# Optimization experiments

Measured on AMD Instinct MI355X. Metric: run time of the kernel, lower is better.

## Reference

```python
import jax, jax.numpy as jnp
import numpy as np

T = 2048          # tokens (single-sequence prefill)
HID = 4096        # hidden_size
NH = 32           # num attention heads
NKV = 8           # num kv heads (GQA)
HD = 128          # head_dim
QKV_OUT = (NH + 2 * NKV) * HD  # 6144
THETA = 10000.0
SCALING = HD ** -0.5


def setup_inputs() -> dict:
    key = jax.random.key(0)
    ks = jax.random.split(key, 8)
    positions = jnp.arange(T, dtype=jnp.int32)
    # per-token int8 quantized hidden states (symmetric, [-127,127])
    q_act = jax.random.randint(ks[0], (T, HID), -127, 128, dtype=jnp.int32)
    # per-token dynamic activation scale
    act_scale = jax.random.uniform(ks[1], (T,), jnp.float32) * 0.01 + 0.001
    # int4 weights stored unsigned [0,15] with per-output-channel scale & zero point
    w_qkv_q = jax.random.randint(ks[2], (QKV_OUT, HID), 0, 16, dtype=jnp.int32)
    w_qkv_scale = jax.random.uniform(ks[3], (QKV_OUT,), jnp.float32) * 0.01 + 0.001
    w_qkv_zero = jax.random.uniform(ks[4], (QKV_OUT,), jnp.float32) * 2.0 + 7.0
    w_o_q = jax.random.randint(ks[5], (HID, HID), 0, 16, dtype=jnp.int32)
    w_o_scale = jax.random.uniform(ks[6], (HID,), jnp.float32) * 0.01 + 0.001
    w_o_zero = jax.random.uniform(ks[7], (HID,), jnp.float32) * 2.0 + 7.0
    return dict(positions=positions, q_act=q_act, act_scale=act_scale,
                w_qkv_q=w_qkv_q, w_qkv_scale=w_qkv_scale, w_qkv_zero=w_qkv_zero,
                w_o_q=w_o_q, w_o_scale=w_o_scale, w_o_zero=w_o_zero)


def w4a8_linear(qa_f, s_a, a_sum, qw, s_w, z_w):
    # y[t,o] = s_a[t]*s_w[o] * ( (qa @ qw^T)[t,o] - z_w[o]*sum_j qa[t,j] )
    acc = jnp.matmul(qa_f, qw.astype(jnp.float32).T)  # [T, O]
    return (s_a[:, None] * s_w[None, :]) * (acc - z_w[None, :] * a_sum[:, None])


def apply_rope(x, positions):
    # neox-style RoPE over full head_dim
    half = HD // 2
    inv_freq = THETA ** (-jnp.arange(0, half, dtype=jnp.float32) / half * 1.0)
    inv_freq = 1.0 / (THETA ** (jnp.arange(0, HD, 2, dtype=jnp.float32) / HD))
    freqs = positions.astype(jnp.float32)[:, None] * inv_freq[None, :]  # [T, HD/2]
    cos = jnp.cos(freqs)[:, None, :]
    sin = jnp.sin(freqs)[:, None, :]
    x1, x2 = x[..., :half], x[..., half:]
    return jnp.concatenate([x1 * cos - x2 * sin, x2 * cos + x1 * sin], axis=-1)


def dynamic_quant_with_sum(x):
    # per-token symmetric int8 dynamic quantization + fused sum
    s = jnp.maximum(jnp.max(jnp.abs(x), axis=-1), 1e-8) / 127.0  # [T]
    q = jnp.clip(jnp.round(x / s[:, None]), -127, 127)
    return q, s, jnp.sum(q, axis=-1)


def reference(positions, q_act, act_scale, w_qkv_q, w_qkv_scale, w_qkv_zero,
              w_o_q, w_o_scale, w_o_zero):
    qa_f = q_act.astype(jnp.float32)
    a_sum = jnp.sum(qa_f, axis=-1)  # fused activation sum
    qkv = w4a8_linear(qa_f, act_scale, a_sum, w_qkv_q, w_qkv_scale, w_qkv_zero)
    q, k, v = jnp.split(qkv, [NH * HD, NH * HD + NKV * HD], axis=-1)
    q = q.reshape(T, NH, HD)
    k = k.reshape(T, NKV, HD)
    v = v.reshape(T, NKV, HD)
    q = apply_rope(q, positions)
    k = apply_rope(k, positions)
    # GQA: repeat kv heads
    rep = NH // NKV
    k = jnp.repeat(k, rep, axis=1)  # [T, NH, HD]
    v = jnp.repeat(v, rep, axis=1)
    scores = jnp.einsum('qhd,khd->hqk', q, k) * SCALING  # [NH, T, T]
    causal = jnp.tril(jnp.ones((T, T), dtype=bool))
    scores = jnp.where(causal[None], scores, -jnp.inf)
    probs = jax.nn.softmax(scores, axis=-1)
    attn = jnp.einsum('hqk,khd->qhd', probs, v).reshape(T, NH * HD)
    # invoke_quant_fuse_sum: dynamic per-token quantization of attn output
    q2, s2, sum2 = dynamic_quant_with_sum(attn)
    out = w4a8_linear(q2, s2, sum2, w_o_q, w_o_scale, w_o_zero)
    return out
```

## Files before the change

kernel.cpp:

```cpp
#include <hip/hip_runtime.h>

#define T 2048
#define HID 4096
#define NH 32
#define NKV 8
#define HD 128
#define QKV_OUT ((NH + 2*NKV) * HD)
#define SCALING 0.08838834764831843f
#define ROPE_C 0.20762050593046014f

typedef __attribute__((ext_vector_type(8))) short bfrag;
typedef __attribute__((ext_vector_type(4))) float ffrag;
typedef __attribute__((ext_vector_type(4))) int  ifrag;
typedef __attribute__((ext_vector_type(16))) char c16;

__device__ __forceinline__ short f2bf(float f) {
  unsigned u = __builtin_bit_cast(unsigned, f);
  u += 0x7fffu + ((u >> 16) & 1u);
  return (short)(u >> 16);
}

__device__ __forceinline__ void split2(float x, short& hi, short& lo) {
  unsigned u = __builtin_bit_cast(unsigned, x);
  unsigned uh = u + (0x7fffu + ((u >> 16) & 1u));
  hi = (short)(uh >> 16);
  float fh = __builtin_bit_cast(float, uh & 0xffff0000u);
  float r = x - fh;
  unsigned ur = __builtin_bit_cast(unsigned, r);
  ur += 0x7fffu + ((ur >> 16) & 1u);
  lo = (short)(ur >> 16);
}

__device__ __forceinline__ void gload_lds16(const void* g, void* l) {
  __builtin_amdgcn_global_load_lds(
      (const __attribute__((address_space(1))) unsigned int*)g,
      (__attribute__((address_space(3))) unsigned int*)l, 16, 0, 0);
}

__global__ __launch_bounds__(256)
void asum_conv(const int* __restrict__ qact, float* __restrict__ a_sum,
               char* __restrict__ a_i8) {
  __shared__ int red[256];
  const int t = blockIdx.x, tid = threadIdx.x;
  const int* row = qact + (size_t)t * HID + tid * 16;
  int s = 0;
  c16 o;
#pragma unroll
  for (int i = 0; i < 4; i++) {
    int4 v = *(const int4*)(row + i * 4);
    s += v.x + v.y + v.z + v.w;
    o[i*4+0] = (char)v.x; o[i*4+1] = (char)v.y;
    o[i*4+2] = (char)v.z; o[i*4+3] = (char)v.w;
  }
  *(c16*)(a_i8 + (size_t)t * HID + tid * 16) = o;
  red[tid] = s; __syncthreads();
  for (int off = 128; off > 0; off >>= 1) {
    if (tid < off) red[tid] += red[tid + off];
    __syncthreads();
  }
  if (tid == 0) a_sum[t] = (float)red[0];
}

__global__ __launch_bounds__(256)
void conv_i2c(const int* __restrict__ src, char* __restrict__ dst, int n16) {
  int idx = blockIdx.x * 256 + threadIdx.x;
  if (idx >= n16) return;
  const int4* s4 = (const int4*)src + (size_t)idx * 4;
  c16 o;
#pragma unroll
  for (int j = 0; j < 4; j++) {
    int4 v = s4[j];
    o[j*4+0] = (char)v.x; o[j*4+1] = (char)v.y;
    o[j*4+2] = (char)v.z; o[j*4+3] = (char)v.w;
  }
  *(c16*)(dst + (size_t)idx * 16) = o;
}

__global__ __launch_bounds__(256)
void gemm_i8(const char* __restrict__ A, const char* __restrict__ W,
             const float* __restrict__ s_a, const float* __restrict__ asum,
             const float* __restrict__ s_w, const float* __restrict__ z_w,
             float* __restrict__ C, int M, int N, int K) {
  __shared__ __align__(16) char As[128 * 64];
  __shared__ __align__(16) char Bs[128 * 64];
  const int tid = threadIdx.x;
  const int lane = tid & 63;
  const int quad = lane >> 4, l15 = lane & 15;
  const int wave = tid >> 6;
  const int wm = (wave >> 1) * 64, wn = (wave & 1) * 64;
  const int bm = blockIdx.y * 128, bn = blockIdx.x * 128;
  const int sr = tid >> 2, sc = (tid & 3) * 16;

  ifrag acc[4][4];
#pragma unroll
  for (int mi = 0; mi < 4; mi++)
#pragma unroll
    for (int ni = 0; ni < 4; ni++)
      acc[mi][ni] = (ifrag){0, 0, 0, 0};

  for (int k0 = 0; k0 < K; k0 += 64) {
#pragma unroll
    for (int it = 0; it < 2; it++) {
      gload_lds16(A + (size_t)(bm + it * 64 + sr) * K + k0 + sc,
                  &As[it * 4096 + wave * 1024]);
      gload_lds16(W + (size_t)(bn + it * 64 + sr) * K + k0 + sc,
                  &Bs[it * 4096 + wave * 1024]);
    }
    __syncthreads();

    ifrag af[4], bfv[4];
#pragma unroll
    for (int mi = 0; mi < 4; mi++)
      af[mi] = *(const ifrag*)&As[(wm + mi * 16 + l15) * 64 + quad * 16];
#pragma unroll
    for (int ni = 0; ni < 4; ni++)
      bfv[ni] = *(const ifrag*)&Bs[(wn + ni * 16 + l15) * 64 + quad * 16];
#pragma unroll
    for (int mi = 0; mi < 4; mi++)
#pragma unroll
      for (int ni = 0; ni < 4; ni++)
        acc[mi][ni] = __builtin_amdgcn_mfma_i32_16x16x64_i8(
            af[mi], bfv[ni], acc[mi][ni], 0, 0, 0);
    __syncthreads();
  }

#pragma unroll
  for (int mi = 0; mi < 4; mi++) {
    int row0 = bm + wm + mi * 16 + quad * 4;
#pragma unroll
    for (int r = 0; r < 4; r++) {
      int row = row0 + r;
      float sa = s_a[row], av = asum[row];
#pragma unroll
      for (int ni = 0; ni < 4; ni++) {
        int col = bn + wn + ni * 16 + l15;
        C[(size_t)row * N + col] = (sa * s_w[col]) * ((float)acc[mi][ni][r] - z_w[col] * av);
      }
    }
  }
}

__global__ __launch_bounds__(256)
void split_kv(float* __restrict__ qkv, const int* __restrict__ positions,
              short* __restrict__ Kh, short* __restrict__ Kl,
              short* __restrict__ Vth) {
  __shared__ __align__(16) short Vh_lds[128 * 72];
  const int y = blockIdx.y;
  const int t0 = blockIdx.x * 64;
  const int tid = threadIdx.x;

  if (y >= NKV) {
    const int h = y - NKV;
#pragma unroll
    for (int it = 0; it < 4; it++) {
      int c = tid + 256 * it;
      int key = c >> 4, dc = c & 15;
      float* qr = qkv + (size_t)(t0 + key) * QKV_OUT + (size_t)h * HD;
      float4 a = *(const float4*)(qr + dc * 4);
      float4 b = *(const float4*)(qr + dc * 4 + 64);
      float av[4] = {a.x, a.y, a.z, a.w};
      float bv[4] = {b.x, b.y, b.z, b.w};
      float pos = (float)positions[t0 + key];
#pragma unroll
      for (int jj = 0; jj < 4; jj++) {
        float fr = pos * exp2f(-ROPE_C * (float)(dc * 4 + jj));
        float sn, cs; sincosf(fr, &sn, &cs);
        float x1 = av[jj], x2 = bv[jj];
        av[jj] = x1 * cs - x2 * sn;
        bv[jj] = x2 * cs + x1 * sn;
      }
      *(float4*)(qr + dc * 4)      = make_float4(av[0], av[1], av[2], av[3]);
      *(float4*)(qr + dc * 4 + 64) = make_float4(bv[0], bv[1], bv[2], bv[3]);
    }
    return;
  }

  const int kvh = y;
#pragma unroll
  for (int it = 0; it < 4; it++) {
    int c = tid + 256 * it;
    int key = c >> 4, dc = c & 15;
    const float* kr = qkv + (size_t)(t0 + key) * QKV_OUT
                      + (size_t)NH * HD + (size_t)kvh * HD;
    float4 a = *(const float4*)(kr + dc * 4);
    float4 b = *(const float4*)(kr + dc * 4 + 64);
    float av[4] = {a.x, a.y, a.z, a.w};
    float bv[4] = {b.x, b.y, b.z, b.w};
    float pos = (float)positions[t0 + key];
    short4 ha, la, hb, lb;
    short hh, ll;
#pragma unroll
    for (int jj = 0; jj < 4; jj++) {
      float fr = pos * exp2f(-ROPE_C * (float)(dc * 4 + jj));
      float sn, cs; sincosf(fr, &sn, &cs);
      float x1 = av[jj], x2 = bv[jj];
      float r1 = x1 * cs - x2 * sn;
      float r2 = x2 * cs + x1 * sn;
      split2(r1, hh, ll); ((short*)&ha)[jj] = hh; ((short*)&la)[jj] = ll;
      split2(r2, hh, ll); ((short*)&hb)[jj] = hh; ((short*)&lb)[jj] = ll;
    }
    size_t o1 = (size_t)kvh * T * HD + (size_t)(t0 + key) * HD + dc * 4;
    *(short4*)(Kh + o1) = ha;      *(short4*)(Kl + o1) = la;
    *(short4*)(Kh + o1 + 64) = hb; *(short4*)(Kl + o1 + 64) = lb;
  }
#pragma unroll
  for (int i = 0; i < 8; i++) {
    int c = tid + 256 * i;
    int key = c >> 5, dc = c & 31;
    float4 f = *(const float4*)(qkv + (size_t)(t0 + key) * QKV_OUT
                                + (size_t)(NH + NKV) * HD + (size_t)kvh * HD + dc * 4);
    Vh_lds[(dc*4+0)*72 + key] = f2bf(f.x);
    Vh_lds[(dc*4+1)*72 + key] = f2bf(f.y);
    Vh_lds[(dc*4+2)*72 + key] = f2bf(f.z);
    Vh_lds[(dc*4+3)*72 + key] = f2bf(f.w);
  }
  __syncthreads();
#pragma unroll
  for (int i = 0; i < 2; i++) {
    int c = tid + 256 * i;
    int row = c >> 2, cc = c & 3;
    size_t o = (size_t)kvh * HD * T + (size_t)row * T + t0 + cc * 8;
    *(bfrag*)(Vth + o) = *(const bfrag*)&Vh_lds[row * 72 + cc * 8];
  }
#pragma unroll
  for (int i = 0; i < 2; i++) {
    int c = tid + 256 * i;
    int row = c >> 2, cc = c & 3;
    size_t o = (size_t)kvh * HD * T + (size_t)row * T + t0 + 32 + cc * 8;
    *(bfrag*)(Vth + o) = *(const bfrag*)&Vh_lds[row * 72 + 32 + cc * 8];
  }
}

__global__ __launch_bounds__(256)
void attn_kernel(const float* __restrict__ qkv,
                 const short* __restrict__ Kh, const short* __restrict__ Kl,
                 const short* __restrict__ Vth,
                 float* __restrict__ Opart, float* __restrict__ Mp,
                 float* __restrict__ Lp, float* __restrict__ attn) {
  __shared__ __align__(16) short Ksh[32 * 136];
  __shared__ __align__(16) short Ksl[32 * 136];
  __shared__ __align__(16) short Vsh[128 * 40];
  __shared__ __align__(16) short Psh[4 * 16 * 40];

  const int kvh = blockIdx.y;
  const int pair = blockIdx.x >> 1;
  const int half = blockIdx.x & 1;
  const int tid = threadIdx.x;
  const int lane = tid & 63;
  const int wv = tid >> 6;
  const int l15 = lane & 15, quad = lane >> 4;
  const int h = kvh * 4 + wv;
  short* Pw = Psh + wv * 16 * 40;

  const short* KhB = Kh + (size_t)kvh * T * HD;
  const short* KlB = Kl + (size_t)kvh * T * HD;
  const short* VhB = Vth + (size_t)kvh * HD * T;

  const int kr = tid >> 4, kc8 = (tid & 15) * 8;
  const int vd = tid >> 2, vc8 = (tid & 3) * 8;

  bfrag rkh0, rkh1, rkl0, rkl1, rv0, rv1;
  auto preload = [&](int k0) {
    rkh0 = *(const bfrag*)(KhB + (size_t)(k0 + kr) * HD + kc8);
    rkh1 = *(const bfrag*)(KhB + (size_t)(k0 + kr + 16) * HD + kc8);
    rkl0 = *(const bfrag*)(KlB + (size_t)(k0 + kr) * HD + kc8);
    rkl1 = *(const bfrag*)(KlB + (size_t)(k0 + kr + 16) * HD + kc8);
    rv0  = *(const bfrag*)(VhB + (size_t)vd * T + k0 + vc8);
    rv1  = *(const bfrag*)(VhB + (size_t)(vd + 64) * T + k0 + vc8);
  };
  preload(half * 32);

  bfrag ones;
#pragma unroll
  for (int j = 0; j < 8; j++) ones[j] = (short)0x3f80;

  for (int pass = 0; pass < 2; pass++) {
    const int qt = pass ? pair : 127 - pair;
    const int q0 = qt * 16;
    const int nk = (q0 >> 5) + 1;

    bfrag qh[4], ql[4];
    const float* qrow = qkv + (size_t)(q0 + l15) * QKV_OUT + (size_t)h * HD;
#pragma unroll
    for (int kc = 0; kc < 4; kc++) {
      float4 f0 = *(const float4*)(qrow + kc * 32 + quad * 8);
      float4 f1 = *(const float4*)(qrow + kc * 32 + quad * 8 + 4);
      float fv[8] = {f0.x, f0.y, f0.z, f0.w, f1.x, f1.y, f1.z, f1.w};
#pragma unroll
      for (int j = 0; j < 8; j++) {
        short hi, lo; split2(fv[j], hi, lo);
        qh[kc][j] = hi; ql[kc][j] = lo;
      }
    }

    ffrag o[8], ol;
    ol = (ffrag){0.f, 0.f, 0.f, 0.f};
#pragma unroll
    for (int n = 0; n < 8; n++) o[n] = (ffrag){0.f, 0.f, 0.f, 0.f};
    float m_i[4] = {-1e30f, -1e30f, -1e30f, -1e30f};

    for (int kt = half; kt < nk; kt += 2) {
      const int k0 = kt << 5;
      __syncthreads();
      *(bfrag*)&Ksh[kr * 136 + kc8] = rkh0;
      *(bfrag*)&Ksh[(kr + 16) * 136 + kc8] = rkh1;
      *(bfrag*)&Ksl[kr * 136 + kc8] = rkl0;
      *(bfrag*)&Ksl[(kr + 16) * 136 + kc8] = rkl1;
      *(bfrag*)&Vsh[vd * 40 + vc8] = rv0;
      *(bfrag*)&Vsh[(vd + 64) * 40 + vc8] = rv1;
      if (kt + 2 < nk) preload(k0 + 64);
      else if (pass == 0) preload(half * 32);
      __syncthreads();

      ffrag s[2];
      s[0] = (ffrag){0.f,0.f,0.f,0.f}; s[1] = (ffrag){0.f,0.f,0.f,0.f};
#pragma unroll
      for (int n = 0; n < 2; n++) {
#pragma unroll
        for (int kc = 0; kc < 4; kc++) {
          bfrag bh = *(const bfrag*)&Ksh[(n*16 + l15) * 136 + kc*32 + quad*8];
          bfrag bl = *(const bfrag*)&Ksl[(n*16 + l15) * 136 + kc*32 + quad*8];
          s[n] = __builtin_amdgcn_mfma_f32_16x16x32_bf16(qh[kc], bh, s[n], 0,0,0);
          s[n] = __builtin_amdgcn_mfma_f32_16x16x32_bf16(qh[kc], bl, s[n], 0,0,0);
          s[n] = __builtin_amdgcn_mfma_f32_16x16x32_bf16(ql[kc], bh, s[n], 0,0,0);
        }
      }
      const bool last = (kt == nk - 1);
      float sv[2][4];
#pragma unroll
      for (int n = 0; n < 2; n++)
#pragma unroll
        for (int r = 0; r < 4; r++) {
          float v = s[n][r] * SCALING;
          if (last) {
            int key = k0 + n * 16 + l15;
            int row = q0 + quad * 4 + r;
            if (key > row) v = -1e30f;
          }
          sv[n][r] = v;
        }
      float alpha[4];
      bool anyup = false;
#pragma unroll
      for (int r = 0; r < 4; r++) {
        float mt = fmaxf(sv[0][r], sv[1][r]);
        mt = fmaxf(mt, __shfl_xor(mt, 1));
        mt = fmaxf(mt, __shfl_xor(mt, 2));
        mt = fmaxf(mt, __shfl_xor(mt, 4));
        mt = fmaxf(mt, __shfl_xor(mt, 8));
        float m_new = fmaxf(m_i[r], mt);
        alpha[r] = __expf(m_i[r] - m_new);
        if (m_new > m_i[r]) anyup = true;
        m_i[r] = m_new;
      }
#pragma unroll
      for (int n = 0; n < 2; n++)
#pragma unroll
        for (int r = 0; r < 4; r++) {
          float p = __expf(sv[n][r] - m_i[r]);
          Pw[(quad*4 + r) * 40 + n*16 + l15] = f2bf(p);
        }
      if (__any(anyup)) {
#pragma unroll
        for (int r = 0; r < 4; r++) ol[r] *= alpha[r];
#pragma unroll
        for (int n = 0; n < 8; n++)
#pragma unroll
          for (int r = 0; r < 4; r++) o[n][r] *= alpha[r];
      }
      bfrag ph = *(const bfrag*)&Pw[l15 * 40 + quad * 8];
      ol = __builtin_amdgcn_mfma_f32_16x16x32_bf16(ph, ones, ol, 0,0,0);
#pragma unroll
      for (int n = 0; n < 8; n++) {
        bfrag vh = *(const bfrag*)&Vsh[(n*16 + l15) * 40 + quad * 8];
        o[n] = __builtin_amdgcn_mfma_f32_16x16x32_bf16(ph, vh, o[n], 0,0,0);
      }
    }

    float* dst = half ? attn : Opart;
#pragma unroll
    for (int n = 0; n < 8; n++)
#pragma unroll
      for (int r = 0; r < 4; r++) {
        int row = q0 + quad * 4 + r;
        dst[(size_t)row * HID + (size_t)h * HD + n * 16 + l15] = o[n][r];
      }
    if (l15 == 0) {
#pragma unroll
      for (int r = 0; r < 4; r++) {
        int row = q0 + quad * 4 + r;
        size_t ix = (size_t)half * NH * T + (size_t)h * T + row;
        Mp[ix] = m_i[r];
        Lp[ix] = ol[r];
      }
    }
  }
}

__global__ __launch_bounds__(256)
void attn_combine(const float* __restrict__ Opart, const float* __restrict__ Mp,
                  const float* __restrict__ Lp, float* attn) {
  const int row = blockIdx.x, tid = threadIdx.x;
  const int h = tid >> 3;
  const float m0 = Mp[(size_t)h * T + row];
  const float m1 = Mp[(size_t)NH * T + (size_t)h * T + row];
  const float l0 = Lp[(size_t)h * T + row];
  const float l1 = Lp[(size_t)NH * T + (size_t)h * T + row];
  const float m = fmaxf(m0, m1);
  float s0 = __expf(m0 - m), s1 = __expf(m1 - m);
  const float inv = 1.f / (l0 * s0 + l1 * s1);
  s0 *= inv; s1 *= inv;
  const size_t base = (size_t)row * HID + (size_t)tid * 16;
  float4* dst = (float4*)(attn + base);
  const float4* p0 = (const float4*)(Opart + base);
#pragma unroll
  for (int i = 0; i < 4; i++) {
    float4 a = p0[i];
    float4 b = dst[i];
    dst[i] = make_float4(a.x * s0 + b.x * s1, a.y * s0 + b.y * s1,
                         a.z * s0 + b.z * s1, a.w * s0 + b.w * s1);
  }
}

__global__ __launch_bounds__(256)
void quant_kernel(const float* __restrict__ x, char* __restrict__ q2,
                  float* __restrict__ s2, float* __restrict__ sum2) {
  __shared__ float red[256];
  const int t = blockIdx.x, tid = threadIdx.x;
  const float* row = x + (size_t)t * HID;
  float4 v[4];
  float m = 0.f;
#pragma unroll
  for (int i = 0; i < 4; i++) {
    v[i] = *(const float4*)(row + tid * 16 + i * 4);
    m = fmaxf(m, fmaxf(fmaxf(fabsf(v[i].x), fabsf(v[i].y)),
                       fmaxf(fabsf(v[i].z), fabsf(v[i].w))));
  }
  red[tid] = m; __syncthreads();
  for (int off = 128; off > 0; off >>= 1) {
    if (tid < off) red[tid] = fmaxf(red[tid], red[tid + off]);
    __syncthreads();
  }
  float s = fmaxf(red[0], 1e-8f) / 127.f;
  __syncthreads();
  float ssum = 0.f;
  c16 o;
#pragma unroll
  for (int i = 0; i < 4; i++) {
    float q;
    q = fminf(127.f, fmaxf(-127.f, rintf(v[i].x / s))); ssum += q; o[i*4+0] = (char)(int)q;
    q = fminf(127.f, fmaxf(-127.f, rintf(v[i].y / s))); ssum += q; o[i*4+1] = (char)(int)q;
    q = fminf(127.f, fmaxf(-127.f, rintf(v[i].z / s))); ssum += q; o[i*4+2] = (char)(int)q;
    q = fminf(127.f, fmaxf(-127.f, rintf(v[i].w / s))); ssum += q; o[i*4+3] = (char)(int)q;
  }
  *(c16*)(q2 + (size_t)t * HID + tid * 16) = o;
  red[tid] = ssum; __syncthreads();
  for (int off = 128; off > 0; off >>= 1) {
    if (tid < off) red[tid] += red[tid + off];
    __syncthreads();
  }
  if (tid == 0) { s2[t] = s; sum2[t] = red[0]; }
}

extern "C" void kernel_launch(void* const* d_in, const int* in_sizes, int n_in,
                              void* d_out, int out_size, void* d_ws, size_t ws_size,
                              hipStream_t stream) {
  const int*   positions   = (const int*)d_in[0];
  const int*   q_act       = (const int*)d_in[1];
  const float* act_scale   = (const float*)d_in[2];
  const int*   w_qkv_q     = (const int*)d_in[3];
  const float* w_qkv_scale = (const float*)d_in[4];
  const float* w_qkv_zero  = (const float*)d_in[5];
  const int*   w_o_q       = (const int*)d_in[6];
  const float* w_o_scale   = (const float*)d_in[7];
  const float* w_o_zero    = (const float*)d_in[8];
  float* out = (float*)d_out;

  size_t off = 0;
  auto alloc = [&](size_t bytes) -> void* {
    void* p = (char*)d_ws + off;
    off += (bytes + 255) & ~(size_t)255;
    return p;
  };
  float* qkv   = (float*)alloc((size_t)T * QKV_OUT * 4);
  char*  act8  = (char*)alloc((size_t)T * HID);
  char*  w8    = (char*)alloc((size_t)QKV_OUT * HID);
  short* Kh    = (short*)alloc((size_t)NKV * T * HD * 2);
  short* Kl    = (short*)alloc((size_t)NKV * T * HD * 2);
  short* Vth   = (short*)alloc((size_t)NKV * T * HD * 2);
  float* a_sum = (float*)alloc(T * 4);
  float* s2    = (float*)alloc(T * 4);
  float* sum2  = (float*)alloc(T * 4);
  float* Mp    = (float*)alloc((size_t)2 * NH * T * 4);
  float* Lp    = (float*)alloc((size_t)2 * NH * T * 4);
  float* Opart = (float*)act8;
  (void)ws_size;

  asum_conv<<<T, 256, 0, stream>>>(q_act, a_sum, act8);
  conv_i2c<<<(QKV_OUT * HID / 16 + 255) / 256, 256, 0, stream>>>(
      w_qkv_q, w8, QKV_OUT * HID / 16);
  gemm_i8<<<dim3(QKV_OUT / 128, T / 128), 256, 0, stream>>>(
      act8, w8, act_scale, a_sum, w_qkv_scale, w_qkv_zero, qkv, T, QKV_OUT, HID);
  split_kv<<<dim3(T / 64, NKV + NH), 256, 0, stream>>>(qkv, positions, Kh, Kl, Vth);
  attn_kernel<<<dim3(128, NKV), 256, 0, stream>>>(
      qkv, Kh, Kl, Vth, Opart, Mp, Lp, out);
  attn_combine<<<T, 256, 0, stream>>>(Opart, Mp, Lp, out);
  conv_i2c<<<(HID * HID / 16 + 255) / 256, 256, 0, stream>>>(
      w_o_q, w8, HID * HID / 16);
  quant_kernel<<<T, 256, 0, stream>>>(out, act8, s2, sum2);
  gemm_i8<<<dim3(HID / 128, T / 128), 256, 0, stream>>>(
      act8, w8, s2, sum2, w_o_scale, w_o_zero, out, T, HID, HID);
}
```

Before: 562.8 us.

## Split attention grid per q-tile, fold scaling into log2 domain, defer rescaling

Each attention block now handles a single 16-row query tile instead of a paired long/short tile, which doubles the grid to 256x8 blocks for more parallelism at the cost of less even per-block work. Q is prescaled by SCALING*log2(e) so that exp2f replaces __expf and the per-score multiply goes away. The online-softmax rescale of the accumulators now happens only when the tile max exceeds the running max by a threshold, which trades some fp32 overflow headroom for fewer rescales. The Q low-part fragments move to LDS to reduce register pressure.

```diff
diff --git a/kernel.cpp b/kernel.cpp
--- a/kernel.cpp
+++ b/kernel.cpp
@@ -7,6 +7,8 @@
 #define HD 128
 #define QKV_OUT ((NH + 2*NKV) * HD)
 #define SCALING 0.08838834764831843f
+#define QS2 0.12751744954f
+#define DEFER_THR 10.0f
 #define ROPE_C 0.20762050593046014f
 
 typedef __attribute__((ext_vector_type(8))) short bfrag;
@@ -241,9 +243,10 @@
   __shared__ __align__(16) short Ksl[32 * 136];
   __shared__ __align__(16) short Vsh[128 * 40];
   __shared__ __align__(16) short Psh[4 * 16 * 40];
+  __shared__ __align__(16) short Qlo[4 * 4 * 512];
 
   const int kvh = blockIdx.y;
-  const int pair = blockIdx.x >> 1;
+  const int qt  = 127 - (int)(blockIdx.x >> 1);
   const int half = blockIdx.x & 1;
   const int tid = threadIdx.x;
   const int lane = tid & 63;
@@ -274,125 +277,126 @@
 #pragma unroll
   for (int j = 0; j < 8; j++) ones[j] = (short)0x3f80;
 
-  for (int pass = 0; pass < 2; pass++) {
-    const int qt = pass ? pair : 127 - pair;
-    const int q0 = qt * 16;
-    const int nk = (q0 >> 5) + 1;
-
-    bfrag qh[4], ql[4];
-    const float* qrow = qkv + (size_t)(q0 + l15) * QKV_OUT + (size_t)h * HD;
+  const int q0 = qt * 16;
+  const int nk = (q0 >> 5) + 1;
+
+  bfrag qh[4];
+  const float* qrow = qkv + (size_t)(q0 + l15) * QKV_OUT + (size_t)h * HD;
+#pragma unroll
+  for (int kc = 0; kc < 4; kc++) {
+    float4 f0 = *(const float4*)(qrow + kc * 32 + quad * 8);
+    float4 f1 = *(const float4*)(qrow + kc * 32 + quad * 8 + 4);
+    float fv[8] = {f0.x, f0.y, f0.z, f0.w, f1.x, f1.y, f1.z, f1.w};
+    bfrag qhv, qlv;
+#pragma unroll
+    for (int j = 0; j < 8; j++) {
+      short hi, lo; split2(fv[j] * QS2, hi, lo);
+      qhv[j] = hi; qlv[j] = lo;
+    }
+    qh[kc] = qhv;
+    *(bfrag*)&Qlo[(wv * 4 + kc) * 512 + lane * 8] = qlv;
+  }
+
+  ffrag o[8], ol;
+  ol = (ffrag){0.f, 0.f, 0.f, 0.f};
+#pragma unroll
+  for (int n = 0; n < 8; n++) o[n] = (ffrag){0.f, 0.f, 0.f, 0.f};
+  float m_i[4] = {-1e30f, -1e30f, -1e30f, -1e30f};
+
+  for (int kt = half; kt < nk; kt += 2) {
+    const int k0 = kt << 5;
+    __syncthreads();
+    *(bfrag*)&Ksh[kr * 136 + kc8] = rkh0;
+    *(bfrag*)&Ksh[(kr + 16) * 136 + kc8] = rkh1;
+    *(bfrag*)&Ksl[kr * 136 + kc8] = rkl0;
+    *(bfrag*)&Ksl[(kr + 16) * 136 + kc8] = rkl1;
+    *(bfrag*)&Vsh[vd * 40 + vc8] = rv0;
+    *(bfrag*)&Vsh[(vd + 64) * 40 + vc8] = rv1;
+    if (kt + 2 < nk) preload(k0 + 64);
+    __syncthreads();
+
+    ffrag s[2];
+    s[0] = (ffrag){0.f,0.f,0.f,0.f}; s[1] = (ffrag){0.f,0.f,0.f,0.f};
 #pragma unroll
     for (int kc = 0; kc < 4; kc++) {
-      float4 f0 = *(const float4*)(qrow + kc * 32 + quad * 8);
-      float4 f1 = *(const float4*)(qrow + kc * 32 + quad * 8 + 4);
-      float fv[8] = {f0.x, f0.y, f0.z, f0.w, f1.x, f1.y, f1.z, f1.w};
-#pragma unroll
-      for (int j = 0; j < 8; j++) {
-        short hi, lo; split2(fv[j], hi, lo);
-        qh[kc][j] = hi; ql[kc][j] = lo;
+      bfrag qlv = *(const bfrag*)&Qlo[(wv * 4 + kc) * 512 + lane * 8];
+#pragma unroll
+      for (int n = 0; n < 2; n++) {
+        bfrag bh = *(const bfrag*)&Ksh[(n*16 + l15) * 136 + kc*32 + quad*8];
+        bfrag bl = *(const bfrag*)&Ksl[(n*16 + l15) * 136 + kc*32 + quad*8];
+        s[n] = __builtin_amdgcn_mfma_f32_16x16x32_bf16(qh[kc], bh, s[n], 0,0,0);
+        s[n] = __builtin_amdgcn_mfma_f32_16x16x32_bf16(qh[kc], bl, s[n], 0,0,0);
+        s[n] = __builtin_amdgcn_mfma_f32_16x16x32_bf16(qlv,    bh, s[n], 0,0,0);
       }
     }
-
-    ffrag o[8], ol;
-    ol = (ffrag){0.f, 0.f, 0.f, 0.f};
-#pragma unroll
-    for (int n = 0; n < 8; n++) o[n] = (ffrag){0.f, 0.f, 0.f, 0.f};
-    float m_i[4] = {-1e30f, -1e30f, -1e30f, -1e30f};
-
-    for (int kt = half; kt < nk; kt += 2) {
-      const int k0 = kt << 5;
-      __syncthreads();
-      *(bfrag*)&Ksh[kr * 136 + kc8] = rkh0;
-      *(bfrag*)&Ksh[(kr + 16) * 136 + kc8] = rkh1;
-      *(bfrag*)&Ksl[kr * 136 + kc8] = rkl0;
-      *(bfrag*)&Ksl[(kr + 16) * 136 + kc8] = rkl1;
-      *(bfrag*)&Vsh[vd * 40 + vc8] = rv0;
-      *(bfrag*)&Vsh[(vd + 64) * 40 + vc8] = rv1;
-      if (kt + 2 < nk) preload(k0 + 64);
-      else if (pass == 0) preload(half * 32);
-      __syncthreads();
-
-      ffrag s[2];
-      s[0] = (ffrag){0.f,0.f,0.f,0.f}; s[1] = (ffrag){0.f,0.f,0.f,0.f};
-#pragma unroll
-      for (int n = 0; n < 2; n++) {
-#pragma unroll
-        for (int kc = 0; kc < 4; kc++) {
-          bfrag bh = *(const bfrag*)&Ksh[(n*16 + l15) * 136 + kc*32 + quad*8];
-          bfrag bl = *(const bfrag*)&Ksl[(n*16 + l15) * 136 + kc*32 + quad*8];
-          s[n] = __builtin_amdgcn_mfma_f32_16x16x32_bf16(qh[kc], bh, s[n], 0,0,0);
-          s[n] = __builtin_amdgcn_mfma_f32_16x16x32_bf16(qh[kc], bl, s[n], 0,0,0);
-          s[n] = __builtin_amdgcn_mfma_f32_16x16x32_bf16(ql[kc], bh, s[n], 0,0,0);
+    const bool lastkt = (kt == nk - 1);
+    float sv[2][4];
+#pragma unroll
+    for (int n = 0; n < 2; n++)
+#pragma unroll
+      for (int r = 0; r < 4; r++) {
+        float v = s[n][r];
+        if (lastkt) {
+          int key = k0 + n * 16 + l15;
+          int row = q0 + quad * 4 + r;
+          if (key > row) v = -1e30f;
         }
+        sv[n][r] = v;
       }
-      const bool last = (kt == nk - 1);
-      float sv[2][4];
-#pragma unroll
-      for (int n = 0; n < 2; n++)
-#pragma unroll
-        for (int r = 0; r < 4; r++) {
-          float v = s[n][r] * SCALING;
-          if (last) {
-            int key = k0 + n * 16 + l15;
-            int row = q0 + quad * 4 + r;
-            if (key > row) v = -1e30f;
-          }
-          sv[n][r] = v;
-        }
-      float alpha[4];
-      bool anyup = false;
+    float mt[4];
+    bool trig = false;
+#pragma unroll
+    for (int r = 0; r < 4; r++) {
+      float m2 = fmaxf(sv[0][r], sv[1][r]);
+      m2 = fmaxf(m2, __shfl_xor(m2, 1));
+      m2 = fmaxf(m2, __shfl_xor(m2, 2));
+      m2 = fmaxf(m2, __shfl_xor(m2, 4));
+      m2 = fmaxf(m2, __shfl_xor(m2, 8));
+      mt[r] = m2;
+      trig = trig || (m2 > m_i[r] + DEFER_THR);
+    }
+    if (__any(trig)) {
 #pragma unroll
       for (int r = 0; r < 4; r++) {
-        float mt = fmaxf(sv[0][r], sv[1][r]);
-        mt = fmaxf(mt, __shfl_xor(mt, 1));
-        mt = fmaxf(mt, __shfl_xor(mt, 2));
-        mt = fmaxf(mt, __shfl_xor(mt, 4));
-        mt = fmaxf(mt, __shfl_xor(mt, 8));
-        float m_new = fmaxf(m_i[r], mt);
-        alpha[r] = __expf(m_i[r] - m_new);
-        if (m_new > m_i[r]) anyup = true;
-        m_i[r] = m_new;
+        float mn = fmaxf(m_i[r], mt[r]);
+        float a = exp2f(m_i[r] - mn);
+        m_i[r] = mn;
+        ol[r] *= a;
+#pragma unroll
+        for (int n = 0; n < 8; n++) o[n][r] *= a;
       }
-#pragma unroll
-      for (int n = 0; n < 2; n++)
-#pragma unroll
-        for (int r = 0; r < 4; r++) {
-          float p = __expf(sv[n][r] - m_i[r]);
-          Pw[(quad*4 + r) * 40 + n*16 + l15] = f2bf(p);
-        }
-      if (__any(anyup)) {
-#pragma unroll
-        for (int r = 0; r < 4; r++) ol[r] *= alpha[r];
-#pragma unroll
-        for (int n = 0; n < 8; n++)
-#pragma unroll
-          for (int r = 0; r < 4; r++) o[n][r] *= alpha[r];
+    }
+#pragma unroll
+    for (int n = 0; n < 2; n++)
+#pragma unroll
+      for (int r = 0; r < 4; r++) {
+        float p = exp2f(sv[n][r] - m_i[r]);
+        Pw[(quad*4 + r) * 40 + n*16 + l15] = f2bf(p);
       }
-      bfrag ph = *(const bfrag*)&Pw[l15 * 40 + quad * 8];
-      ol = __builtin_amdgcn_mfma_f32_16x16x32_bf16(ph, ones, ol, 0,0,0);
-#pragma unroll
-      for (int n = 0; n < 8; n++) {
-        bfrag vh = *(const bfrag*)&Vsh[(n*16 + l15) * 40 + quad * 8];
-        o[n] = __builtin_amdgcn_mfma_f32_16x16x32_bf16(ph, vh, o[n], 0,0,0);
-      }
-    }
-
-    float* dst = half ? attn : Opart;
-#pragma unroll
-    for (int n = 0; n < 8; n++)
-#pragma unroll
-      for (int r = 0; r < 4; r++) {
-        int row = q0 + quad * 4 + r;
-        dst[(size_t)row * HID + (size_t)h * HD + n * 16 + l15] = o[n][r];
-      }
-    if (l15 == 0) {
-#pragma unroll
-      for (int r = 0; r < 4; r++) {
-        int row = q0 + quad * 4 + r;
-        size_t ix = (size_t)half * NH * T + (size_t)h * T + row;
-        Mp[ix] = m_i[r];
-        Lp[ix] = ol[r];
-      }
+    bfrag ph = *(const bfrag*)&Pw[l15 * 40 + quad * 8];
+    ol = __builtin_amdgcn_mfma_f32_16x16x32_bf16(ph, ones, ol, 0,0,0);
+#pragma unroll
+    for (int n = 0; n < 8; n++) {
+      bfrag vh = *(const bfrag*)&Vsh[(n*16 + l15) * 40 + quad * 8];
+      o[n] = __builtin_amdgcn_mfma_f32_16x16x32_bf16(ph, vh, o[n], 0,0,0);
+    }
+  }
+
+  float* dst = half ? attn : Opart;
+#pragma unroll
+  for (int n = 0; n < 8; n++)
+#pragma unroll
+    for (int r = 0; r < 4; r++) {
+      int row = q0 + quad * 4 + r;
+      dst[(size_t)row * HID + (size_t)h * HD + n * 16 + l15] = o[n][r];
+    }
+  if (l15 == 0) {
+#pragma unroll
+    for (int r = 0; r < 4; r++) {
+      int row = q0 + quad * 4 + r;
+      size_t ix = (size_t)half * NH * T + (size_t)h * T + row;
+      Mp[ix] = m_i[r];
+      Lp[ix] = ol[r];
     }
   }
 }
@@ -407,7 +411,7 @@
   const float l0 = Lp[(size_t)h * T + row];
   const float l1 = Lp[(size_t)NH * T + (size_t)h * T + row];
   const float m = fmaxf(m0, m1);
-  float s0 = __expf(m0 - m), s1 = __expf(m1 - m);
+  float s0 = exp2f(m0 - m), s1 = exp2f(m1 - m);
   const float inv = 1.f / (l0 * s0 + l1 * s1);
   s0 *= inv; s1 *= inv;
   const size_t base = (size_t)row * HID + (size_t)tid * 16;
@@ -502,7 +506,7 @@
   gemm_i8<<<dim3(QKV_OUT / 128, T / 128), 256, 0, stream>>>(
       act8, w8, act_scale, a_sum, w_qkv_scale, w_qkv_zero, qkv, T, QKV_OUT, HID);
   split_kv<<<dim3(T / 64, NKV + NH), 256, 0, stream>>>(qkv, positions, Kh, Kl, Vth);
-  attn_kernel<<<dim3(128, NKV), 256, 0, stream>>>(
+  attn_kernel<<<dim3(256, NKV), 256, 0, stream>>>(
       qkv, Kh, Kl, Vth, Opart, Mp, Lp, out);
   attn_combine<<<T, 256, 0, stream>>>(Opart, Mp, Lp, out);
   conv_i2c<<<(HID * HID / 16 + 255) / 256, 256, 0, stream>>>(
```

New measurement: 599.9 us. +6.6%, slower.
